# Kernel tuning notes

Measured on AMD Instinct MI355X. Metric: run time of the kernel, lower is better.

## Reference

```python
import jax, jax.numpy as jnp
import numpy as np

D_MODEL = 1024
D_HIDDEN = 4096
N_EXPERTS = 8
B, S = 2, 2048


def setup_inputs() -> dict:
    key = jax.random.key(0)
    ks = jax.random.split(key, 4)
    sd = 1.0 / np.sqrt(D_MODEL)
    sh = 1.0 / np.sqrt(D_HIDDEN)
    return {
        "x": jax.random.normal(ks[0], (B, S, D_MODEL), dtype=jnp.float32),
        "Wg": jax.random.normal(ks[1], (D_MODEL, N_EXPERTS), dtype=jnp.float32) * sd,
        "bg": jnp.zeros((N_EXPERTS,), dtype=jnp.float32),
        "W1": jax.random.normal(ks[2], (N_EXPERTS, D_MODEL, D_HIDDEN), dtype=jnp.float32) * sd,
        "b1": jnp.zeros((N_EXPERTS, D_HIDDEN), dtype=jnp.float32),
        "W2": jax.random.normal(ks[3], (N_EXPERTS, D_HIDDEN, D_MODEL), dtype=jnp.float32) * sh,
        "b2": jnp.zeros((N_EXPERTS, D_MODEL), dtype=jnp.float32),
    }


def reference(x, Wg, bg, W1, b1, W2, b2):
    # Router: softmax is monotone, so argmax(softmax(logits)) == argmax(logits).
    logits = jnp.einsum("bsd,de->bse", x, Wg) + bg
    expert_idx = jnp.argmax(logits, axis=-1)  # [B, S]
    # Top-1 dispatch, expressed as compute-all-experts + per-token select
    # (jit-friendly; the torch loop masks/gathers per expert).
    h = jax.nn.gelu(jnp.einsum("bsd,edh->bseh", x, W1) + b1, approximate=False)
    y = jnp.einsum("bseh,ehd->bsed", h, W2) + b2  # [B, S, E, D]
    out = jnp.take_along_axis(y, expert_idx[:, :, None, None], axis=2)[:, :, 0, :]
    return out
```

## Files before the change

kernel.cpp:

```cpp
#include <hip/hip_runtime.h>
#include <hip/hip_bf16.h>
#include <math.h>

#define D_MODEL 1024
#define D_HIDDEN 4096
#define N_EXP 8
#define N_TOK 4096
#define MBS2 24

typedef __attribute__((ext_vector_type(8))) __bf16 bf16x8_t;
typedef __attribute__((ext_vector_type(4))) float f32x4_t;

#define WS_PREFIX_OFF 128
#define WS_BUCKET_OFF 256
#define WS_HT_OFF     ((size_t)1 << 18)
#define WS_XB_OFF     ((size_t)1 << 18)
#define WS_HFB_OFF    (((size_t)1 << 18) + ((size_t)8 << 20))
#define WS_W1T_OFF    (((size_t)1 << 18) + ((size_t)48 << 20))
#define WS_W2T_OFF    (((size_t)1 << 18) + ((size_t)112 << 20))
#define WS_AE_OFF     (((size_t)1 << 18) + ((size_t)176 << 20))
#define WS_NEED       (((size_t)1 << 18) + ((size_t)188 << 20))

__device__ __forceinline__ void gload16(const void* g, void* l) {
    __builtin_amdgcn_global_load_lds(
        (__attribute__((address_space(1))) void*)(g),
        (__attribute__((address_space(3))) void*)(l),
        16, 0, 0);
}

__global__ __launch_bounds__(64) void init_counts(int* counts) {
    if (threadIdx.x < N_EXP) counts[threadIdx.x] = 0;
}

__global__ __launch_bounds__(64) void prefix_kernel(const int* counts, int* prefix) {
    if (threadIdx.x == 0) {
        int s = 0;
        prefix[0] = 0;
#pragma unroll
        for (int e = 0; e < N_EXP; ++e) { s += (counts[e] + 255) >> 8; prefix[e + 1] = s; }
    }
}

__global__ __launch_bounds__(256) void router_kernel(
    const float* __restrict__ x, const float* __restrict__ Wg,
    const float* __restrict__ bg, int* __restrict__ counts,
    int* __restrict__ bucket, __hip_bfloat16* __restrict__ xb)
{
    const int wid  = threadIdx.x >> 6;
    const int lane = threadIdx.x & 63;
    const int t    = blockIdx.x * 4 + wid;
    const float* xr = x + (size_t)t * D_MODEL;

    double acc[N_EXP];
#pragma unroll
    for (int e = 0; e < N_EXP; ++e) acc[e] = 0.0;

#pragma unroll
    for (int j = 0; j < D_MODEL / 64; ++j) {
        const int d = j * 64 + lane;
        const float xv = xr[d];
        xb[(size_t)t * D_MODEL + d] = __float2bfloat16(xv);
        const float4* wr = (const float4*)(Wg + (size_t)d * N_EXP);
        const float4 w0 = wr[0], w1 = wr[1];
        const double xd = (double)xv;
        acc[0] += xd * (double)w0.x; acc[1] += xd * (double)w0.y;
        acc[2] += xd * (double)w0.z; acc[3] += xd * (double)w0.w;
        acc[4] += xd * (double)w1.x; acc[5] += xd * (double)w1.y;
        acc[6] += xd * (double)w1.z; acc[7] += xd * (double)w1.w;
    }
#pragma unroll
    for (int e = 0; e < N_EXP; ++e) {
        double v = acc[e];
#pragma unroll
        for (int off = 32; off >= 1; off >>= 1) v += __shfl_xor(v, off, 64);
        acc[e] = v + (double)bg[e];
    }
    if (lane == 0) {
        int best = 0; double bv = acc[0];
#pragma unroll
        for (int e = 1; e < N_EXP; ++e)
            if (acc[e] > bv) { bv = acc[e]; best = e; }
        const int pos = atomicAdd(&counts[best], 1);
        bucket[best * N_TOK + pos] = t;
    }
}

template<int KT, int NT>
__global__ __launch_bounds__(256) void convert_w(
    const float* __restrict__ W, __hip_bfloat16* __restrict__ Wt)
{
    constexpr int NB = NT / 256, KC = KT / 64;
    const int nb128 = blockIdx.x, kc = blockIdx.y, e = blockIdx.z;
    const int k0 = kc * 64, n0 = nb128 * 128;
    const int nb = n0 >> 8, halfc = (n0 >> 7) & 1;
    const int tid = threadIdx.x;
    __shared__ __hip_bfloat16 Lt[128 * 68];

    const int nq  = tid & 31;
    const int kq2 = tid >> 5;
#pragma unroll
    for (int h = 0; h < 2; ++h) {
        const int kq = kq2 + h * 8;
        const float* src = W + (size_t)e * KT * NT + (size_t)(k0 + kq * 4) * NT + n0 + nq * 4;
        const float4 v0 = *(const float4*)(src);
        const float4 v1 = *(const float4*)(src + (size_t)NT);
        const float4 v2 = *(const float4*)(src + (size_t)2 * NT);
        const float4 v3 = *(const float4*)(src + (size_t)3 * NT);
#pragma unroll
        for (int i = 0; i < 4; ++i) {
            const int n = nq * 4 + i;
            union { __hip_bfloat16 hh[4]; unsigned long long u; } pk;
            pk.hh[0] = __float2bfloat16(((const float*)&v0)[i]);
            pk.hh[1] = __float2bfloat16(((const float*)&v1)[i]);
            pk.hh[2] = __float2bfloat16(((const float*)&v2)[i]);
            pk.hh[3] = __float2bfloat16(((const float*)&v3)[i]);
            *(unsigned long long*)((char*)Lt + (size_t)n * 136 + kq * 8) = pk.u;
        }
    }
    __syncthreads();

    char* outc = (char*)Wt + (((size_t)e * NB + nb) * KC + kc) * 32768 + halfc * 16384;
    const int n = tid >> 1, half = tid & 1;
#pragma unroll
    for (int s = 0; s < 4; ++s) {
        const int slot = half * 4 + s;
        const int ko = slot ^ (n & 7);
        const uint4 v = *(const uint4*)((const char*)Lt + (size_t)n * 136 + ko * 16);
        *(uint4*)(outc + (size_t)n * 128 + slot * 16) = v;
    }
}

__global__ __launch_bounds__(256) void gather_a(
    const float* __restrict__ x, const int* __restrict__ counts,
    const int* __restrict__ prefix, const int* __restrict__ bucket,
    __hip_bfloat16* __restrict__ Ae)
{
    const int mbg = blockIdx.x >> 1, halfm = blockIdx.x & 1, kc = blockIdx.y;
    if (mbg >= prefix[8]) return;
    int e = 0;
#pragma unroll
    for (int q = 1; q < 8; ++q) if (mbg >= prefix[q]) e = q;
    const int cnt  = counts[e];
    const int mblk = mbg - prefix[e];
    const int tid  = threadIdx.x;
    const int m = halfm * 128 + (tid >> 1);
    const int half = tid & 1;
    int idx = mblk * 256 + m;
    if (idx >= cnt) idx = cnt - 1;
    const int tok = bucket[e * N_TOK + idx];
    const float* src = x + (size_t)tok * D_MODEL + kc * 64 + half * 32;
    char* dst = (char*)Ae + ((size_t)mbg * 16 + kc) * 32768 + (size_t)m * 128;
#pragma unroll
    for (int s = 0; s < 4; ++s) {
        const float4 a = *(const float4*)(src + s * 8);
        const float4 b = *(const float4*)(src + s * 8 + 4);
        union { __hip_bfloat16 hh[8]; uint4 u; } pk;
#pragma unroll
        for (int j = 0; j < 4; ++j) {
            pk.hh[j]     = __float2bfloat16(((const float*)&a)[j]);
            pk.hh[j + 4] = __float2bfloat16(((const float*)&b)[j]);
        }
        const int ko = half * 4 + s;
        *(uint4*)(dst + ((ko ^ (m & 7)) << 4)) = pk.u;
    }
}

template<int K_TOT, int N_TOT, int SPLITS, bool IS_FFN1>
__global__ __launch_bounds__(512, 2) void ffn_gemm_q(
    const __hip_bfloat16* __restrict__ At,
    const __hip_bfloat16* __restrict__ Wt,
    const float* __restrict__ bias,
    const int* __restrict__ prefix,
    __hip_bfloat16* __restrict__ hout,
    float* __restrict__ pout)
{
    constexpr int KC     = K_TOT / 64;
    constexpr int KSTEPS = KC / SPLITS;
    constexpr int NB     = N_TOT / 256;
    constexpr int NWG    = NB * SPLITS * MBS2;

    const int orig = blockIdx.x;
    const int wg   = (orig & 7) * (NWG >> 3) + (orig >> 3);
    const int nblk = wg / (SPLITS * MBS2);
    const int r2   = wg % (SPLITS * MBS2);
    const int split = r2 / MBS2;
    const int mbg   = r2 % MBS2;
    if (mbg >= prefix[8]) return;
    int e = 0;
#pragma unroll
    for (int q = 1; q < 8; ++q) if (mbg >= prefix[q]) e = q;
    const int n0 = nblk * 256;

    const int tid  = threadIdx.x;
    const int lane = tid & 63;
    const int wid  = tid >> 6;
    const int wm   = wid >> 1, wn = wid & 1;

    __shared__ char As[32768];
    __shared__ char Bs[32768];

    const char* Ab = (const char*)At + ((size_t)mbg * KC + split * KSTEPS) * 32768;
    const char* Bb = (const char*)Wt + (((size_t)e * NB + nblk) * KC + split * KSTEPS) * 32768;
    const int off = wid * 4096 + lane * 16;
    char* lA = As + wid * 4096;
    char* lB = Bs + wid * 4096;

    f32x4_t acc[4][8];
#pragma unroll
    for (int f = 0; f < 4; ++f)
#pragma unroll
        for (int g = 0; g < 8; ++g) acc[f][g] = (f32x4_t){0.f, 0.f, 0.f, 0.f};

    for (int t = 0; t < KSTEPS; ++t) {
        const char* Ac = Ab + (size_t)t * 32768 + off;
        const char* Bc = Bb + (size_t)t * 32768 + off;
#pragma unroll
        for (int i = 0; i < 4; ++i) gload16(Ac + i * 1024, lA + i * 1024);
#pragma unroll
        for (int i = 0; i < 4; ++i) gload16(Bc + i * 1024, lB + i * 1024);
        __syncthreads();

#pragma unroll
        for (int kk = 0; kk < 2; ++kk) {
            uint4 af[4], bf[8];
            const int ko = kk * 4 + (lane >> 4);
#pragma unroll
            for (int f = 0; f < 4; ++f) {
                const int r = wm * 64 + f * 16 + (lane & 15);
                af[f] = *(const uint4*)(As + r * 128 + ((ko ^ (r & 7)) << 4));
            }
#pragma unroll
            for (int g = 0; g < 8; ++g) {
                const int n = wn * 128 + g * 16 + (lane & 15);
                bf[g] = *(const uint4*)(Bs + n * 128 + ((ko ^ (n & 7)) << 4));
            }
#pragma unroll
            for (int f = 0; f < 4; ++f)
#pragma unroll
                for (int g = 0; g < 8; ++g)
                    acc[f][g] = __builtin_amdgcn_mfma_f32_16x16x32_bf16(
                        __builtin_bit_cast(bf16x8_t, af[f]),
                        __builtin_bit_cast(bf16x8_t, bf[g]),
                        acc[f][g], 0, 0, 0);
        }
        __syncthreads();
    }

    if (IS_FFN1) {
        char* hb = (char*)hout + (size_t)mbg * (D_HIDDEN / 64) * 32768;
#pragma unroll
        for (int f = 0; f < 4; ++f) {
#pragma unroll
            for (int j = 0; j < 4; ++j) {
                const int m = wm * 64 + f * 16 + (lane >> 4) * 4 + j;
#pragma unroll
                for (int g = 0; g < 8; ++g) {
                    const int col = n0 + wn * 128 + g * 16 + (lane & 15);
                    float v = acc[f][g][j] + bias[e * N_TOT + col];
                    v = 0.5f * v * (1.0f + erff(v * 0.70710678118654752f));
                    const int kc = col >> 6, kw = col & 63, ko = kw >> 3, b = kw & 7;
                    *(__hip_bfloat16*)(hb + (size_t)kc * 32768 + (size_t)m * 128 +
                                       (((ko ^ (m & 7)) << 4) + (b << 1))) = __float2bfloat16(v);
                }
            }
        }
    } else {
        float* pb = pout + ((size_t)(split * MBS2 + mbg) * 256) * 1024;
#pragma unroll
        for (int f = 0; f < 4; ++f) {
#pragma unroll
            for (int j = 0; j < 4; ++j) {
                const int m = wm * 64 + f * 16 + (lane >> 4) * 4 + j;
#pragma unroll
                for (int g = 0; g < 8; ++g) {
                    const int col = n0 + wn * 128 + g * 16 + (lane & 15);
                    pb[(size_t)m * 1024 + col] = acc[f][g][j];
                }
            }
        }
    }
}

__global__ __launch_bounds__(256) void reduce_out(
    const float* __restrict__ P, const float* __restrict__ b2,
    const int* __restrict__ counts, const int* __restrict__ prefix,
    const int* __restrict__ bucket, float* __restrict__ out)
{
    const int slot = blockIdx.x;
    if (slot >= prefix[8]) return;
    int e = 0;
#pragma unroll
    for (int q = 1; q < 8; ++q) if (slot >= prefix[q]) e = q;
    const int cnt  = counts[e];
    const int mblk = slot - prefix[e];
    const int r    = blockIdx.y * 4 + (threadIdx.x >> 6);
    const int idx  = mblk * 256 + r;
    if (idx >= cnt) return;
    const int tok  = bucket[e * N_TOK + idx];
    const int lane = threadIdx.x & 63;
    const float* p0 = P + ((size_t)slot * 256 + r) * 1024;
    const float* p1 = P + ((size_t)(MBS2 + slot) * 256 + r) * 1024;
    const float* bb = b2 + e * 1024;
    float* op = out + (size_t)tok * 1024;
#pragma unroll
    for (int j = 0; j < 4; ++j) {
        const int c = j * 256 + lane * 4;
        const float4 a = *(const float4*)(p0 + c);
        const float4 b = *(const float4*)(p1 + c);
        const float4 w = *(const float4*)(bb + c);
        float4 v;
        v.x = a.x + b.x + w.x; v.y = a.y + b.y + w.y;
        v.z = a.z + b.z + w.z; v.w = a.w + b.w + w.w;
        *(float4*)(op + c) = v;
    }
}

template<int K_TOT, int N_TOT, bool IS_FFN1>
__global__ __launch_bounds__(256, 2) void ffn_gemm_f32(
    const __hip_bfloat16* __restrict__ A,
    const float* __restrict__ W,
    const float* __restrict__ bias,
    const int* __restrict__ counts,
    const int* __restrict__ bucket,
    __hip_bfloat16* __restrict__ hout,
    float* __restrict__ yout)
{
    const int e   = blockIdx.z;
    const int cnt = counts[e];
    const int m0  = blockIdx.y * 128;
    if (m0 >= cnt) return;
    const int n0   = blockIdx.x * 128;
    const int tid  = threadIdx.x;
    const int lane = tid & 63;
    const int wid  = tid >> 6;
    const int wm   = wid >> 1, wn = wid & 1;

    __shared__ __hip_bfloat16 As[128 * 64];
    __shared__ __hip_bfloat16 Bs[128 * 64];
    __shared__ int s_tok[128];

    if (tid < 128) {
        int idx = m0 + tid;
        if (idx >= cnt) idx = cnt - 1;
        s_tok[tid] = bucket[e * N_TOK + idx];
    }
    __syncthreads();

    const __hip_bfloat16* gA[4]; char* lA[4];
#pragma unroll
    for (int i = 0; i < 4; ++i) {
        const int r = wid * 32 + i * 8 + (lane >> 3);
        gA[i] = A + (size_t)s_tok[r] * K_TOT + (((lane & 7) ^ (r & 7)) << 3);
        lA[i] = (char*)As + (size_t)(wid * 32 + i * 8) * 128;
    }
    const int ko_t = lane & 7;
    const int nq   = wid * 8 + (lane >> 3);
    const float* wb = W + (size_t)e * K_TOT * N_TOT + (size_t)(ko_t * 8) * N_TOT + n0 + nq * 4;

    f32x4_t acc[4][4];
#pragma unroll
    for (int f = 0; f < 4; ++f)
#pragma unroll
        for (int g = 0; g < 4; ++g) acc[f][g] = (f32x4_t){0.f, 0.f, 0.f, 0.f};

    for (int k0 = 0; k0 < K_TOT; k0 += 64) {
#pragma unroll
        for (int i = 0; i < 4; ++i) gload16(gA[i] + k0, lA[i]);
        const float* wk = wb + (size_t)k0 * N_TOT;
        float4 v[8];
#pragma unroll
        for (int j = 0; j < 8; ++j) v[j] = *(const float4*)(wk + (size_t)j * N_TOT);
#pragma unroll
        for (int i = 0; i < 4; ++i) {
            const int n = nq * 4 + i;
            union { __hip_bfloat16 hh[8]; uint4 u; } pk;
#pragma unroll
            for (int j = 0; j < 8; ++j) pk.hh[j] = __float2bfloat16(((const float*)&v[j])[i]);
            *(uint4*)((char*)Bs + n * 128 + ((ko_t ^ (n & 7)) << 4)) = pk.u;
        }
        __syncthreads();

#pragma unroll
        for (int kk = 0; kk < 2; ++kk) {
            uint4 af[4], bf[4];
            const int ko = kk * 4 + (lane >> 4);
#pragma unroll
            for (int f = 0; f < 4; ++f) {
                const int r = wm * 64 + f * 16 + (lane & 15);
                af[f] = *(const uint4*)((const char*)As + r * 128 + ((ko ^ (r & 7)) << 4));
            }
#pragma unroll
            for (int g = 0; g < 4; ++g) {
                const int n = wn * 64 + g * 16 + (lane & 15);
                bf[g] = *(const uint4*)((const char*)Bs + n * 128 + ((ko ^ (n & 7)) << 4));
            }
#pragma unroll
            for (int f = 0; f < 4; ++f)
#pragma unroll
                for (int g = 0; g < 4; ++g)
                    acc[f][g] = __builtin_amdgcn_mfma_f32_16x16x32_bf16(
                        __builtin_bit_cast(bf16x8_t, af[f]),
                        __builtin_bit_cast(bf16x8_t, bf[g]),
                        acc[f][g], 0, 0, 0);
        }
        __syncthreads();
    }

#pragma unroll
    for (int f = 0; f < 4; ++f) {
#pragma unroll
        for (int j = 0; j < 4; ++j) {
            const int rl = wm * 64 + f * 16 + (lane >> 4) * 4 + j;
            const bool ok = (m0 + rl) < cnt;
            const int tok = s_tok[rl];
#pragma unroll
            for (int g = 0; g < 4; ++g) {
                const int col = n0 + wn * 64 + g * 16 + (lane & 15);
                float v = acc[f][g][j] + bias[e * N_TOT + col];
                if (IS_FFN1) {
                    v = 0.5f * v * (1.0f + erff(v * 0.70710678118654752f));
                    if (ok) hout[(size_t)tok * N_TOT + col] = __float2bfloat16(v);
                } else {
                    if (ok) yout[(size_t)tok * N_TOT + col] = v;
                }
            }
        }
    }
}

extern "C" void kernel_launch(void* const* d_in, const int* in_sizes, int n_in,
                              void* d_out, int out_size, void* d_ws, size_t ws_size,
                              hipStream_t stream) {
    const float* x  = (const float*)d_in[0];
    const float* Wg = (const float*)d_in[1];
    const float* bg = (const float*)d_in[2];
    const float* W1 = (const float*)d_in[3];
    const float* b1 = (const float*)d_in[4];
    const float* W2 = (const float*)d_in[5];
    const float* b2 = (const float*)d_in[6];
    float* out = (float*)d_out;

    char* ws = (char*)d_ws;
    int* counts = (int*)(ws);
    int* prefix = (int*)(ws + WS_PREFIX_OFF);
    int* bucket = (int*)(ws + WS_BUCKET_OFF);
    __hip_bfloat16* xb  = (__hip_bfloat16*)(ws + WS_XB_OFF);
    __hip_bfloat16* ht  = (__hip_bfloat16*)(ws + WS_HT_OFF);
    __hip_bfloat16* hfb = (__hip_bfloat16*)(ws + WS_HFB_OFF);
    __hip_bfloat16* w1t = (__hip_bfloat16*)(ws + WS_W1T_OFF);
    __hip_bfloat16* w2t = (__hip_bfloat16*)(ws + WS_W2T_OFF);
    __hip_bfloat16* ae  = (__hip_bfloat16*)(ws + WS_AE_OFF);
    float* partials     = (float*)(ws + WS_W1T_OFF);

    init_counts<<<dim3(1), dim3(64), 0, stream>>>(counts);
    router_kernel<<<dim3(N_TOK / 4), dim3(256), 0, stream>>>(x, Wg, bg, counts, bucket, xb);
    prefix_kernel<<<dim3(1), dim3(64), 0, stream>>>(counts, prefix);

    if (ws_size >= WS_NEED) {
        convert_w<D_MODEL, D_HIDDEN><<<dim3(32, 16, N_EXP), dim3(256), 0, stream>>>(W1, w1t);
        convert_w<D_HIDDEN, D_MODEL><<<dim3(8, 64, N_EXP), dim3(256), 0, stream>>>(W2, w2t);
        gather_a<<<dim3(MBS2 * 2, 16), dim3(256), 0, stream>>>(x, counts, prefix, bucket, ae);
        ffn_gemm_q<D_MODEL, D_HIDDEN, 1, true>
            <<<dim3(MBS2 * (D_HIDDEN / 256)), dim3(512), 0, stream>>>(
                ae, w1t, b1, prefix, ht, nullptr);
        ffn_gemm_q<D_HIDDEN, D_MODEL, 2, false>
            <<<dim3(MBS2 * (D_MODEL / 256) * 2), dim3(512), 0, stream>>>(
                ht, w2t, nullptr, prefix, nullptr, partials);
        reduce_out<<<dim3(MBS2, 64), dim3(256), 0, stream>>>(
            partials, b2, counts, prefix, bucket, out);
    } else {
        ffn_gemm_f32<D_MODEL, D_HIDDEN, true>
            <<<dim3(D_HIDDEN / 128, N_TOK / 128, N_EXP), dim3(256), 0, stream>>>(
                xb, W1, b1, counts, bucket, hfb, nullptr);
        ffn_gemm_f32<D_HIDDEN, D_MODEL, false>
            <<<dim3(D_MODEL / 128, N_TOK / 128, N_EXP), dim3(256), 0, stream>>>(
                hfb, W2, b2, counts, bucket, nullptr, out);
    }
}
```

Baseline: 374.2 us.

## Double-buffer LDS tiles to overlap global loads with MFMA compute

Doubles the A and B shared-memory buffers and prefetches the next K-step tile via global_load_lds while the current tile feeds the MFMAs, with explicit vmcnt waits and barriers at the end of each step. The goal is to hide global memory latency behind matrix math instead of stalling on a barrier before every step. LDS use rises from 64KB to 128KB per block, which can lower occupancy.

```diff
diff --git a/kernel.cpp b/kernel.cpp
--- a/kernel.cpp
+++ b/kernel.cpp
@@ -196,8 +196,8 @@
     const int wid  = tid >> 6;
     const int wm   = wid >> 1, wn = wid & 1;
 
-    __shared__ char As[32768];
-    __shared__ char Bs[32768];
+    __shared__ char As[2 * 32768];
+    __shared__ char Bs[2 * 32768];
 
     const char* Ab = (const char*)At + ((size_t)mbg * KC + split * KSTEPS) * 32768;
     const char* Bb = (const char*)Wt + (((size_t)e * NB + nblk) * KC + split * KSTEPS) * 32768;
@@ -211,15 +211,34 @@
 #pragma unroll
         for (int g = 0; g < 8; ++g) acc[f][g] = (f32x4_t){0.f, 0.f, 0.f, 0.f};
 
+    {
+        const char* Ac = Ab + off;
+        const char* Bc = Bb + off;
+#pragma unroll
+        for (int i = 0; i < 4; ++i) gload16(Ac + i * 1024, lA + i * 1024);
+#pragma unroll
+        for (int i = 0; i < 4; ++i) gload16(Bc + i * 1024, lB + i * 1024);
+    }
+    asm volatile("s_waitcnt vmcnt(0)" ::: "memory");
+    __builtin_amdgcn_s_barrier();
+    __builtin_amdgcn_sched_barrier(0);
+
     for (int t = 0; t < KSTEPS; ++t) {
-        const char* Ac = Ab + (size_t)t * 32768 + off;
-        const char* Bc = Bb + (size_t)t * 32768 + off;
-#pragma unroll
-        for (int i = 0; i < 4; ++i) gload16(Ac + i * 1024, lA + i * 1024);
-#pragma unroll
-        for (int i = 0; i < 4; ++i) gload16(Bc + i * 1024, lB + i * 1024);
-        __syncthreads();
-
+        const int c = t & 1;
+        if (t + 1 < KSTEPS) {
+            const char* Ac = Ab + (size_t)(t + 1) * 32768 + off;
+            const char* Bc = Bb + (size_t)(t + 1) * 32768 + off;
+            char* la = lA + (c ^ 1) * 32768;
+            char* lb = lB + (c ^ 1) * 32768;
+#pragma unroll
+            for (int i = 0; i < 4; ++i) gload16(Ac + i * 1024, la + i * 1024);
+#pragma unroll
+            for (int i = 0; i < 4; ++i) gload16(Bc + i * 1024, lb + i * 1024);
+        }
+        __builtin_amdgcn_sched_barrier(0);
+
+        const char* asb = As + c * 32768;
+        const char* bsb = Bs + c * 32768;
 #pragma unroll
         for (int kk = 0; kk < 2; ++kk) {
             uint4 af[4], bf[8];
@@ -227,12 +246,12 @@
 #pragma unroll
             for (int f = 0; f < 4; ++f) {
                 const int r = wm * 64 + f * 16 + (lane & 15);
-                af[f] = *(const uint4*)(As + r * 128 + ((ko ^ (r & 7)) << 4));
+                af[f] = *(const uint4*)(asb + r * 128 + ((ko ^ (r & 7)) << 4));
             }
 #pragma unroll
             for (int g = 0; g < 8; ++g) {
                 const int n = wn * 128 + g * 16 + (lane & 15);
-                bf[g] = *(const uint4*)(Bs + n * 128 + ((ko ^ (n & 7)) << 4));
+                bf[g] = *(const uint4*)(bsb + n * 128 + ((ko ^ (n & 7)) << 4));
             }
 #pragma unroll
             for (int f = 0; f < 4; ++f)
@@ -243,7 +262,10 @@
                         __builtin_bit_cast(bf16x8_t, bf[g]),
                         acc[f][g], 0, 0, 0);
         }
-        __syncthreads();
+
+        asm volatile("s_waitcnt vmcnt(0)" ::: "memory");
+        __builtin_amdgcn_s_barrier();
+        __builtin_amdgcn_sched_barrier(0);
     }
 
     if (IS_FFN1) {
```

New measurement: 354.8 us. -5.2%, faster.
